# Kernel optimization log

Measured on AMD Instinct MI355X. Metric: run time of the kernel, lower is better.

The kernel has to match this reference:

```python
import jax, jax.numpy as jnp
import numpy as np

B, S, H = 4, 1024, 1024
NH, HD = 16, 64
SCALE = 1.0 / np.sqrt(HD)
VERB_BIAS, ROOT_BIAS, SUFFIX_BIAS = 2.0, 1.5, 1.2
BIG = np.float32(1e9)


def setup_inputs() -> dict:
    key = jax.random.key(0)
    ks = jax.random.split(key, 10)
    inp = {
        "hidden_states": jax.random.normal(ks[0], (B, S, H), dtype=jnp.float32),
        "morpho_types": jax.random.randint(ks[1], (B, S), 0, 5, dtype=jnp.int32),
        # torch Linear: y = x @ W.T + b; store W already transposed as [in, out]
        "Wq": jax.random.normal(ks[2], (H, H), dtype=jnp.float32) * 0.02,
        "bq": jnp.zeros((H,), dtype=jnp.float32),
        "Wk": jax.random.normal(ks[3], (H, H), dtype=jnp.float32) * 0.02,
        "bk": jnp.zeros((H,), dtype=jnp.float32),
        "Wv": jax.random.normal(ks[4], (H, H), dtype=jnp.float32) * 0.02,
        "bv": jnp.zeros((H,), dtype=jnp.float32),
        "Wo": jax.random.normal(ks[5], (H, H), dtype=jnp.float32) * 0.02,
        "bo": jnp.zeros((H,), dtype=jnp.float32),
    }
    return inp


def _morpho_bias(morpho_types):
    """Vectorized equivalent of _create_morpho_bias_mask. Returns [B, S, S]
    (the torch version broadcasts the same bias over all heads)."""
    is_verb = morpho_types == 2                      # [B, S]
    pos = jnp.arange(S)
    dist = jnp.abs(pos[:, None] - pos[None, :])      # [S, S]
    # mask non-verb columns with a huge distance; argmin ties -> smallest j,
    # matching torch's argmin over ascending verb_positions
    dist_m = jnp.where(is_verb[:, None, :], dist[None], BIG)  # [B, S, S]
    nearest = jnp.argmin(dist_m, axis=-1)            # [B, S]
    has_verb = jnp.any(is_verb, axis=-1)             # [B]
    verb_term = VERB_BIAS * jax.nn.one_hot(nearest, S, dtype=jnp.float32)
    verb_term = verb_term * has_verb[:, None, None].astype(jnp.float32)
    col_bias = (ROOT_BIAS * 0.5) * (morpho_types == 0).astype(jnp.float32) \
             + (SUFFIX_BIAS * 0.3) * (morpho_types == 1).astype(jnp.float32)  # [B, S]
    return verb_term + col_bias[:, None, :]          # [B, S, S]


def reference(hidden_states, morpho_types, Wq, bq, Wk, bk, Wv, bv, Wo, bo):
    def proj(W, b):
        y = hidden_states @ W + b                    # [B, S, H]
        return y.reshape(B, S, NH, HD).transpose(0, 2, 1, 3)  # [B, NH, S, HD]

    q = proj(Wq, bq)
    k = proj(Wk, bk)
    v = proj(Wv, bv)

    scores = jnp.einsum('bhqd,bhkd->bhqk', q, k) * SCALE   # [B, NH, S, S]
    scores = scores + _morpho_bias(morpho_types)[:, None]  # broadcast heads

    attn = jax.nn.softmax(scores, axis=-1)
    out = jnp.einsum('bhqk,bhkd->bhqd', attn, v)           # [B, NH, S, HD]
    out = out.transpose(0, 2, 1, 3).reshape(B, S, H)
    return out @ Wo + bo
```

## Files before the change

### kernel.cpp

```cpp
#include <hip/hip_runtime.h>


#define QSCALE 0.18033688011112042f
#define CB0    1.0820212806667225f
#define CB1    0.5193702147200268f
#define VERB2  2.8853900817779268f

typedef float  f32x4   __attribute__((ext_vector_type(4)));
typedef short  s16x8   __attribute__((ext_vector_type(8)));
typedef unsigned short u16x4 __attribute__((ext_vector_type(4)));
typedef unsigned short u16x8 __attribute__((ext_vector_type(8)));

#if __has_builtin(__builtin_amdgcn_exp2f)
#define EXP2F(x) __builtin_amdgcn_exp2f(x)
#else
#define EXP2F(x) exp2f(x)
#endif

__device__ __forceinline__ unsigned short f2bf(float f) {
  union { float f; unsigned u; } a; a.f = f;
  unsigned r = a.u + 0x7fffu + ((a.u >> 16) & 1u);
  return (unsigned short)(r >> 16);
}

__device__ __forceinline__ void async16(const void* g, void* l) {
  __builtin_amdgcn_global_load_lds(
      (const __attribute__((address_space(1))) unsigned int*)g,
      (__attribute__((address_space(3))) unsigned int*)l, 16, 0, 0);
}

__global__ __launch_bounds__(256) void k_prep(
    const float* __restrict__ hs, unsigned short* __restrict__ hsb,
    const float* __restrict__ Wq, const float* __restrict__ Wk,
    const float* __restrict__ Wv, const float* __restrict__ Wo,
    unsigned short* __restrict__ Wt, const int* __restrict__ mt,
    float* __restrict__ colbias, int* __restrict__ nearest) {
  __shared__ float t[64 * 68];
  int bx = blockIdx.x, tid = threadIdx.x;
  if (bx < 2048) {
    int i = (bx * 256 + tid) * 8;
    float4 v0 = *(const float4*)(hs + i);
    float4 v1 = *(const float4*)(hs + i + 4);
    u16x8 o;
    o[0] = f2bf(v0.x); o[1] = f2bf(v0.y); o[2] = f2bf(v0.z); o[3] = f2bf(v0.w);
    o[4] = f2bf(v1.x); o[5] = f2bf(v1.y); o[6] = f2bf(v1.z); o[7] = f2bf(v1.w);
    *(u16x8*)(hsb + i) = o;
  } else if (bx < 3072) {
    int w = (bx - 2048) >> 8, tt = (bx - 2048) & 255;
    const float* W = (w == 0) ? Wq : (w == 1) ? Wk : (w == 2) ? Wv : Wo;
    unsigned short* Wd = Wt + (size_t)w * 1048576;
    int n0 = (tt & 15) * 64, k0 = (tt >> 4) * 64;
    int r = tid >> 2, c0 = (tid & 3) * 16;
    const float* src = &W[(k0 + r) * 1024 + n0 + c0];
    float4 a0 = *(const float4*)(src + 0);
    float4 a1 = *(const float4*)(src + 4);
    float4 a2 = *(const float4*)(src + 8);
    float4 a3 = *(const float4*)(src + 12);
    *(float4*)&t[r * 68 + c0 + 0]  = a0;
    *(float4*)&t[r * 68 + c0 + 4]  = a1;
    *(float4*)&t[r * 68 + c0 + 8]  = a2;
    *(float4*)&t[r * 68 + c0 + 12] = a3;
    __syncthreads();
    u16x8 o0, o1;
#pragma unroll
    for (int j = 0; j < 8; j++) {
      o0[j] = f2bf(t[(c0 + j) * 68 + r]);
      o1[j] = f2bf(t[(c0 + 8 + j) * 68 + r]);
    }
    *(u16x8*)&Wd[(n0 + r) * 1024 + k0 + c0]     = o0;
    *(u16x8*)&Wd[(n0 + r) * 1024 + k0 + c0 + 8] = o1;
  } else {
    int i = bx - 3072;
    int b = i >> 2;
    int* sm = (int*)t;
    for (int j = tid; j < 1024; j += 256) sm[j] = mt[b * 1024 + j];
    __syncthreads();
    int q = (i & 3) * 256 + tid;
    int best = 1 << 30, bj = -1;
    for (int j = 0; j < 1024; ++j) {
      int d = (q > j) ? (q - j) : (j - q);
      int dd = (sm[j] == 2) ? d : (1 << 30);
      if (dd < best) { best = dd; bj = j; }
    }
    nearest[b * 1024 + q] = bj;
    int m = sm[q];
    colbias[b * 1024 + q] = CB0 * (m == 0) + CB1 * (m == 1);
  }
}

template <int MODE>
__global__ __launch_bounds__(256) void k_gemm(
    const unsigned short* __restrict__ A,
    const unsigned short* __restrict__ WtBase,
    const float* __restrict__ bias0, const float* __restrict__ bias1,
    const float* __restrict__ bias2,
    unsigned short* __restrict__ outB, unsigned short* __restrict__ outV,
    float* __restrict__ outF) {
  constexpr int TM = (MODE == 0) ? 128 : 64;
  constexpr int NI = (MODE == 0) ? 4 : 2;
  constexpr int RA = TM / 4;
  __shared__ unsigned short As[TM * 64];
  __shared__ unsigned short Bs[128 * 64];
  int tid = threadIdx.x, wid = tid >> 6, lane = tid & 63;
  int c = lane & 15, quad = lane >> 4;
  int m0, wsel, n0;
  const unsigned short* Bt;
  const float* bias;
  if (MODE == 0) {
    wsel = blockIdx.x >> 3;
    n0 = (blockIdx.x & 7) * 128;
    m0 = blockIdx.y * 128;
    Bt = WtBase + wsel * 1048576;
    bias = (wsel == 0) ? bias0 : ((wsel == 1) ? bias1 : bias2);
  } else {
    wsel = 0;
    n0 = blockIdx.x * 128;
    m0 = blockIdx.y * 64;
    Bt = WtBase; bias = bias0;
  }
  int wm = (wid >> 1) * (16 * NI), wn = (wid & 1) * 64;
  int lr = lane >> 3, lc = lane & 7;
  int gcol = ((lc ^ lr) << 3);
  const unsigned short* ga = A  + (size_t)(m0 + wid * RA + lr) * 1024 + gcol;
  const unsigned short* gb = Bt + (size_t)(n0 + wid * 32 + lr) * 1024 + gcol;
  unsigned short* lA = &As[(wid * RA) * 64];
  unsigned short* lB = &Bs[(wid * 32) * 64];

  f32x4 acc[NI][4];
#pragma unroll
  for (int i = 0; i < NI; i++)
#pragma unroll
    for (int j = 0; j < 4; j++) acc[i][j] = (f32x4){0.f, 0.f, 0.f, 0.f};

  bool sw = (MODE == 1) || (wsel != 2);

  for (int k0 = 0; k0 < 1024; k0 += 64) {
#pragma unroll
    for (int i = 0; i < RA / 8; i++) async16(ga + i * 8 * 1024 + k0, lA + i * 8 * 64);
#pragma unroll
    for (int j = 0; j < 4; j++)      async16(gb + j * 8 * 1024 + k0, lB + j * 8 * 64);
    __syncthreads();
#pragma unroll
    for (int ks = 0; ks < 2; ks++) {
      s16x8 af[NI], bf[4];
#pragma unroll
      for (int i = 0; i < NI; i++)
        af[i] = *(const s16x8*)&As[(wm + i * 16 + c) * 64 + (((ks * 4 + quad) ^ (c & 7)) << 3)];
#pragma unroll
      for (int j = 0; j < 4; j++)
        bf[j] = *(const s16x8*)&Bs[(wn + j * 16 + c) * 64 + (((ks * 4 + quad) ^ (c & 7)) << 3)];
      if (sw) {
#pragma unroll
        for (int i = 0; i < NI; i++)
#pragma unroll
          for (int j = 0; j < 4; j++)
            acc[i][j] = __builtin_amdgcn_mfma_f32_16x16x32_bf16(bf[j], af[i], acc[i][j], 0, 0, 0);
      } else {
#pragma unroll
        for (int i = 0; i < NI; i++)
#pragma unroll
          for (int j = 0; j < 4; j++)
            acc[i][j] = __builtin_amdgcn_mfma_f32_16x16x32_bf16(af[i], bf[j], acc[i][j], 0, 0, 0);
      }
    }
    __syncthreads();
  }

  if (MODE == 1) {
#pragma unroll
    for (int j = 0; j < 4; j++) {
      int colb = n0 + wn + j * 16 + quad * 4;
      f32x4 bvv = *(const f32x4*)&bias[colb];
#pragma unroll
      for (int i = 0; i < NI; i++) {
        int s_tok = m0 + wm + i * 16 + c;
        f32x4 v = acc[i][j] + bvv;
        *(f32x4*)&outF[(size_t)s_tok * 1024 + colb] = v;
      }
    }
  } else if (wsel == 2) {
#pragma unroll
    for (int j = 0; j < 4; j++) {
      int col = n0 + wn + j * 16 + c;
      float bv = bias[col];
      int h = col >> 6, d = col & 63;
#pragma unroll
      for (int i = 0; i < NI; i++) {
        int row = m0 + wm + i * 16 + quad * 4;
        int bb = row >> 10, s = row & 1023;
        u16x4 pk;
#pragma unroll
        for (int r = 0; r < 4; r++) pk[r] = f2bf(acc[i][j][r] + bv);
        *(u16x4*)&outV[(size_t)(((bb * 16 + h) * 64 + d)) * 1024 + s] = pk;
      }
    }
  } else {
    float sc = (wsel == 0) ? QSCALE : 1.0f;
#pragma unroll
    for (int j = 0; j < 4; j++) {
      int colb = n0 + wn + j * 16 + quad * 4;
      f32x4 bvv = *(const f32x4*)&bias[colb];
      int h = colb >> 6, d0 = colb & 63;
#pragma unroll
      for (int i = 0; i < NI; i++) {
        int s_tok = m0 + wm + i * 16 + c;
        int bb = s_tok >> 10, s = s_tok & 1023;
        u16x4 pk;
#pragma unroll
        for (int r = 0; r < 4; r++) pk[r] = f2bf((acc[i][j][r] + bvv[r]) * sc);
        *(u16x4*)&outB[(size_t)wsel * 4194304 + (((bb * 16 + h) * 1024 + s) * 64) + d0] = pk;
      }
    }
  }
}

__global__ __launch_bounds__(256) void k_attn(
    const unsigned short* __restrict__ Q, const unsigned short* __restrict__ K,
    const unsigned short* __restrict__ Vt, const float* __restrict__ colbias,
    const int* __restrict__ nearest, unsigned short* __restrict__ AO) {
  __shared__ unsigned short Ks[64 * 72];
  __shared__ unsigned short Vs[64 * 72];
  __shared__ unsigned short Ps[4][32 * 72];
  __shared__ float Cb[1024];
  int tid = threadIdx.x, wid = tid >> 6, lane = tid & 63;
  int c = lane & 15, quad = lane >> 4;
  int bh = blockIdx.x, qt = blockIdx.y;
  int b = bh >> 4, head = bh & 15;
  int q0 = qt * 128, wq = wid * 32;
  const unsigned short* Qg = Q  + (size_t)(bh * 1024 + q0 + wq) * 64;
  const unsigned short* Kg = K  + (size_t)bh * 1024 * 64;
  const unsigned short* Vg = Vt + (size_t)bh * 64 * 1024;

  *(float4*)&Cb[tid * 4] = *(const float4*)&colbias[b * 1024 + tid * 4];

  s16x8 qf[2][2];
#pragma unroll
  for (int nt = 0; nt < 2; nt++)
#pragma unroll
    for (int ks = 0; ks < 2; ks++)
      qf[nt][ks] = *(const s16x8*)&Qg[(nt * 16 + c) * 64 + ks * 32 + quad * 8];

  int nq[2];
  nq[0] = nearest[b * 1024 + q0 + wq + c];
  nq[1] = nearest[b * 1024 + q0 + wq + 16 + c];

  f32x4 o[2][4];
#pragma unroll
  for (int i = 0; i < 2; i++)
#pragma unroll
    for (int j = 0; j < 4; j++) o[i][j] = (f32x4){0.f, 0.f, 0.f, 0.f};
  float lrun[2] = {0.f, 0.f};

  int srow = tid >> 3, scol8 = (tid & 7) * 8;

  u16x8 kr[2], vr[2];
#pragma unroll
  for (int it = 0; it < 2; ++it) {
    int r2 = it * 32 + srow;
    kr[it] = *(const u16x8*)&Kg[r2 * 64 + scol8];
    vr[it] = *(const u16x8*)&Vg[r2 * 1024 + scol8];
  }
  __syncthreads();

  for (int kc = 0; kc < 16; ++kc) {
#pragma unroll
    for (int it = 0; it < 2; ++it) {
      int r2 = it * 32 + srow;
      *(u16x8*)&Ks[r2 * 72 + scol8] = kr[it];
      *(u16x8*)&Vs[r2 * 72 + scol8] = vr[it];
    }
    __syncthreads();
    if (kc < 15) {
#pragma unroll
      for (int it = 0; it < 2; ++it) {
        int r2 = it * 32 + srow;
        kr[it] = *(const u16x8*)&Kg[((kc + 1) * 64 + r2) * 64 + scol8];
        vr[it] = *(const u16x8*)&Vg[r2 * 1024 + (kc + 1) * 64 + scol8];
      }
    }

    f32x4 st[4][2];
#pragma unroll
    for (int mt = 0; mt < 4; mt++)
#pragma unroll
      for (int nt = 0; nt < 2; nt++) st[mt][nt] = (f32x4){0.f, 0.f, 0.f, 0.f};
#pragma unroll
    for (int mt = 0; mt < 4; mt++)
#pragma unroll
      for (int ks = 0; ks < 2; ks++) {
        s16x8 a = *(const s16x8*)&Ks[(mt * 16 + c) * 72 + ks * 32 + quad * 8];
#pragma unroll
        for (int nt = 0; nt < 2; nt++)
          st[mt][nt] = __builtin_amdgcn_mfma_f32_16x16x32_bf16(a, qf[nt][ks], st[mt][nt], 0, 0, 0);
      }

    bool h0 = (nq[0] >> 6) == kc;
    bool h1 = (nq[1] >> 6) == kc;
    if (__any(h0 || h1)) {
#pragma unroll
      for (int mt = 0; mt < 4; mt++)
#pragma unroll
        for (int nt = 0; nt < 2; nt++)
#pragma unroll
          for (int r = 0; r < 4; r++)
            if (kc * 64 + mt * 16 + quad * 4 + r == nq[nt]) st[mt][nt][r] += VERB2;
    }

#pragma unroll
    for (int mt = 0; mt < 4; mt++) {
      f32x4 cb = *(const f32x4*)&Cb[kc * 64 + mt * 16 + quad * 4];
#pragma unroll
      for (int nt = 0; nt < 2; nt++) {
        float e0 = EXP2F(st[mt][nt][0] + cb[0]);
        float e1 = EXP2F(st[mt][nt][1] + cb[1]);
        float e2 = EXP2F(st[mt][nt][2] + cb[2]);
        float e3 = EXP2F(st[mt][nt][3] + cb[3]);
        unsigned p01 = __builtin_amdgcn_perm(__float_as_uint(e1), __float_as_uint(e0), 0x07060302u);
        unsigned p23 = __builtin_amdgcn_perm(__float_as_uint(e3), __float_as_uint(e2), 0x07060302u);
        lrun[nt] += __uint_as_float(p01 << 16) + __uint_as_float(p01 & 0xffff0000u)
                  + __uint_as_float(p23 << 16) + __uint_as_float(p23 & 0xffff0000u);
        uint2 pk; pk.x = p01; pk.y = p23;
        *(uint2*)&Ps[wid][(nt * 16 + c) * 72 + mt * 16 + quad * 4] = pk;
      }
    }
    __asm__ volatile("s_waitcnt lgkmcnt(0)" ::: "memory");

#pragma unroll
    for (int ks = 0; ks < 2; ks++) {
      s16x8 pa[2];
#pragma unroll
      for (int mtq = 0; mtq < 2; mtq++)
        pa[mtq] = *(const s16x8*)&Ps[wid][(mtq * 16 + c) * 72 + ks * 32 + quad * 8];
#pragma unroll
      for (int ntd = 0; ntd < 4; ntd++) {
        s16x8 vb = *(const s16x8*)&Vs[(ntd * 16 + c) * 72 + ks * 32 + quad * 8];
#pragma unroll
        for (int mtq = 0; mtq < 2; mtq++)
          o[mtq][ntd] = __builtin_amdgcn_mfma_f32_16x16x32_bf16(vb, pa[mtq], o[mtq][ntd], 0, 0, 0);
      }
    }
    __syncthreads();
  }

#pragma unroll
  for (int nt = 0; nt < 2; nt++) {
    lrun[nt] += __shfl_xor(lrun[nt], 16, 64);
    lrun[nt] += __shfl_xor(lrun[nt], 32, 64);
  }
  float linv[2] = {1.0f / lrun[0], 1.0f / lrun[1]};
#pragma unroll
  for (int mtq = 0; mtq < 2; mtq++) {
    size_t row = (size_t)(b * 1024 + q0 + wq + mtq * 16 + c);
#pragma unroll
    for (int ntd = 0; ntd < 4; ntd++) {
      int d0 = ntd * 16 + quad * 4;
      u16x4 pk;
#pragma unroll
      for (int r = 0; r < 4; r++) pk[r] = f2bf(o[mtq][ntd][r] * linv[mtq]);
      *(u16x4*)&AO[row * 1024 + head * 64 + d0] = pk;
    }
  }
}

extern "C" void kernel_launch(void* const* d_in, const int* in_sizes, int n_in,
                              void* d_out, int out_size, void* d_ws, size_t ws_size,
                              hipStream_t stream) {
  const float* hs     = (const float*)d_in[0];
  const int*   morpho = (const int*)d_in[1];
  const float* Wq = (const float*)d_in[2];
  const float* bq = (const float*)d_in[3];
  const float* Wk = (const float*)d_in[4];
  const float* bk = (const float*)d_in[5];
  const float* Wv = (const float*)d_in[6];
  const float* bv = (const float*)d_in[7];
  const float* Wo = (const float*)d_in[8];
  const float* bo = (const float*)d_in[9];
  float* out = (float*)d_out;

  char* ws = (char*)d_ws;
  unsigned short* hsb = (unsigned short*)(ws);
  unsigned short* Wt  = (unsigned short*)(ws + (8u << 20));
  unsigned short* Qb  = (unsigned short*)(ws + (16u << 20));
  unsigned short* Kb  = (unsigned short*)(ws + (24u << 20));
  unsigned short* Vtb = (unsigned short*)(ws + (40u << 20));
  float* colbias      = (float*)(ws + (48u << 20));
  int*   nearestp     = (int*)(ws + (48u << 20) + (16u << 10));
  unsigned short* AO  = hsb;

  k_prep<<<3088, 256, 0, stream>>>(hs, hsb, Wq, Wk, Wv, Wo, Wt, morpho,
                                   colbias, nearestp);
  k_gemm<0><<<dim3(24, 32), 256, 0, stream>>>(hsb, Wt, bq, bk, bv, Qb, Vtb, nullptr);
  k_attn<<<dim3(64, 8), 256, 0, stream>>>(Qb, Kb, Vtb, colbias, nearestp, AO);
  k_gemm<1><<<dim3(8, 64), 256, 0, stream>>>(AO, Wt + 3 * 1048576, bo, nullptr, nullptr,
                                             nullptr, nullptr, out);
  (void)in_sizes; (void)n_in; (void)out_size; (void)ws_size; (void)Kb;
}
```

Baseline: 211.1 us.

## Replace QKV projection GEMM with 256x256-tile 8-wave pipelined kernel

Adds a new QKV projection kernel that uses 256x256 output tiles with 512 threads, double-buffered async global-to-LDS loads with XOR-swizzled layout, and interleaved LDS reads and MFMA quads with barriers and s_setprio. The aim is more data reuse per tile and better overlap of memory traffic with matrix math than the previous 128-wide GEMM. The trade-off is a grid of only 192 blocks, which may underfill the 256 CUs, plus high register pressure from the 8x4 accumulators.

```diff
diff --git a/kernel.cpp b/kernel.cpp
--- a/kernel.cpp
+++ b/kernel.cpp
@@ -214,6 +214,178 @@
   }
 }
 
+#define QKV_QUAD(AFR, MB, NB)                                                 \
+  if (sw) {                                                                   \
+    _Pragma("unroll") for (int ks = 0; ks < 2; ks++)                          \
+    _Pragma("unroll") for (int mf = 0; mf < 4; mf++)                          \
+    _Pragma("unroll") for (int nf = 0; nf < 2; nf++)                          \
+      acc[(MB) + mf][(NB) + nf] = __builtin_amdgcn_mfma_f32_16x16x32_bf16(    \
+          b[(NB) + nf][ks], AFR[mf][ks], acc[(MB) + mf][(NB) + nf], 0, 0, 0); \
+  } else {                                                                    \
+    _Pragma("unroll") for (int ks = 0; ks < 2; ks++)                          \
+    _Pragma("unroll") for (int mf = 0; mf < 4; mf++)                          \
+    _Pragma("unroll") for (int nf = 0; nf < 2; nf++)                          \
+      acc[(MB) + mf][(NB) + nf] = __builtin_amdgcn_mfma_f32_16x16x32_bf16(    \
+          AFR[mf][ks], b[(NB) + nf][ks], acc[(MB) + mf][(NB) + nf], 0, 0, 0); \
+  }
+
+template <bool STAGE, int VMN>
+__device__ __forceinline__ void qkv_ktile(
+    unsigned short* Ac, unsigned short* Bc,
+    const unsigned short* ga, const unsigned short* gb, int k2,
+    int wid, int wm, int wn, int c, int quad, bool sw, f32x4 (&acc)[8][4]) {
+  const int cs = c & 7;
+  s16x8 a0[4][2], a1[4][2], b[4][2];
+#pragma unroll
+  for (int mf = 0; mf < 4; mf++)
+#pragma unroll
+    for (int ks = 0; ks < 2; ks++)
+      a0[mf][ks] = *(const s16x8*)&Ac[(wm * 128 + mf * 16 + c) * 64 + (((ks * 4 + quad) ^ cs) << 3)];
+#pragma unroll
+  for (int nf = 0; nf < 2; nf++)
+#pragma unroll
+    for (int ks = 0; ks < 2; ks++)
+      b[nf][ks] = *(const s16x8*)&Bc[(wn * 64 + nf * 16 + c) * 64 + (((ks * 4 + quad) ^ cs) << 3)];
+  __builtin_amdgcn_s_barrier();
+  __asm__ volatile("s_waitcnt lgkmcnt(0)" ::: "memory");
+  __builtin_amdgcn_s_setprio(1);
+  QKV_QUAD(a0, 0, 0)
+  __builtin_amdgcn_s_setprio(0);
+  __builtin_amdgcn_s_barrier();
+#pragma unroll
+  for (int nf = 2; nf < 4; nf++)
+#pragma unroll
+    for (int ks = 0; ks < 2; ks++)
+      b[nf][ks] = *(const s16x8*)&Bc[(wn * 64 + nf * 16 + c) * 64 + (((ks * 4 + quad) ^ cs) << 3)];
+#pragma unroll
+  for (int mf = 0; mf < 4; mf++)
+#pragma unroll
+    for (int ks = 0; ks < 2; ks++)
+      a1[mf][ks] = *(const s16x8*)&Ac[(wm * 128 + 64 + mf * 16 + c) * 64 + (((ks * 4 + quad) ^ cs) << 3)];
+  __builtin_amdgcn_s_barrier();
+  __asm__ volatile("s_waitcnt lgkmcnt(0)" ::: "memory");
+  __builtin_amdgcn_s_setprio(1);
+  QKV_QUAD(a0, 0, 2)
+  __builtin_amdgcn_s_setprio(0);
+  __builtin_amdgcn_s_barrier();
+  if constexpr (STAGE) {
+#pragma unroll
+    for (int j = 0; j < 2; j++) {
+      async16(ga + j * 8 * 1024 + k2, Ac + (wid * 32 + j * 8) * 64);
+      async16(gb + j * 8 * 1024 + k2, Bc + (wid * 32 + j * 8) * 64);
+    }
+  }
+  __builtin_amdgcn_s_barrier();
+  __builtin_amdgcn_s_setprio(1);
+  QKV_QUAD(a1, 4, 0)
+  __builtin_amdgcn_s_setprio(0);
+  __builtin_amdgcn_s_barrier();
+  if constexpr (STAGE) {
+#pragma unroll
+    for (int j = 2; j < 4; j++) {
+      async16(ga + j * 8 * 1024 + k2, Ac + (wid * 32 + j * 8) * 64);
+      async16(gb + j * 8 * 1024 + k2, Bc + (wid * 32 + j * 8) * 64);
+    }
+  }
+  __builtin_amdgcn_s_barrier();
+  __builtin_amdgcn_s_setprio(1);
+  QKV_QUAD(a1, 4, 2)
+  __builtin_amdgcn_s_setprio(0);
+  if constexpr (VMN == 8)
+    __asm__ volatile("s_waitcnt vmcnt(8)" ::: "memory");
+  else if constexpr (VMN == 0)
+    __asm__ volatile("s_waitcnt vmcnt(0)" ::: "memory");
+  __builtin_amdgcn_s_barrier();
+}
+
+__global__ __launch_bounds__(512, 2) void k_qkv256(
+    const unsigned short* __restrict__ A,
+    const unsigned short* __restrict__ WtBase,
+    const float* __restrict__ bq, const float* __restrict__ bk,
+    const float* __restrict__ bv,
+    unsigned short* __restrict__ outQK, unsigned short* __restrict__ outV) {
+  __shared__ unsigned short As[2][256 * 64];
+  __shared__ unsigned short Bs[2][256 * 64];
+  int tid = threadIdx.x, wid = tid >> 6, lane = tid & 63;
+  int c = lane & 15, quad = lane >> 4;
+  int wm = wid >> 2, wn = wid & 3;
+  int wsel = blockIdx.x >> 2;
+  int n0 = (blockIdx.x & 3) * 256;
+  int m0 = blockIdx.y * 256;
+  const unsigned short* Bt = WtBase + (size_t)wsel * 1048576;
+  const float* bias = (wsel == 0) ? bq : ((wsel == 1) ? bk : bv);
+  bool sw = (wsel != 2);
+
+  int lr = lane >> 3, lc = lane & 7;
+  int gcol = (lc ^ lr) << 3;
+  const unsigned short* ga = A  + (size_t)(m0 + wid * 32 + lr) * 1024 + gcol;
+  const unsigned short* gb = Bt + (size_t)(n0 + wid * 32 + lr) * 1024 + gcol;
+
+  f32x4 acc[8][4];
+#pragma unroll
+  for (int i = 0; i < 8; i++)
+#pragma unroll
+    for (int j = 0; j < 4; j++) acc[i][j] = (f32x4){0.f, 0.f, 0.f, 0.f};
+
+#pragma unroll
+  for (int j = 0; j < 4; j++) {
+    async16(ga + j * 8 * 1024,      &As[0][(wid * 32 + j * 8) * 64]);
+    async16(gb + j * 8 * 1024,      &Bs[0][(wid * 32 + j * 8) * 64]);
+  }
+#pragma unroll
+  for (int j = 0; j < 4; j++) {
+    async16(ga + j * 8 * 1024 + 64, &As[1][(wid * 32 + j * 8) * 64]);
+    async16(gb + j * 8 * 1024 + 64, &Bs[1][(wid * 32 + j * 8) * 64]);
+  }
+  __asm__ volatile("s_waitcnt vmcnt(8)" ::: "memory");
+  __builtin_amdgcn_s_barrier();
+
+  for (int kt = 0; kt < 14; kt += 2) {
+    qkv_ktile<true, 8>(&As[0][0], &Bs[0][0], ga, gb, (kt + 2) * 64,
+                       wid, wm, wn, c, quad, sw, acc);
+    qkv_ktile<true, 8>(&As[1][0], &Bs[1][0], ga, gb, (kt + 3) * 64,
+                       wid, wm, wn, c, quad, sw, acc);
+  }
+  qkv_ktile<false, 0>(&As[0][0], &Bs[0][0], ga, gb, 0, wid, wm, wn, c, quad, sw, acc);
+  qkv_ktile<false, -1>(&As[1][0], &Bs[1][0], ga, gb, 0, wid, wm, wn, c, quad, sw, acc);
+
+  if (!sw) {
+#pragma unroll
+    for (int nf = 0; nf < 4; nf++) {
+      int col = n0 + wn * 64 + nf * 16 + c;
+      float bvv = bias[col];
+      int h = col >> 6, d = col & 63;
+#pragma unroll
+      for (int mf = 0; mf < 8; mf++) {
+        int row = m0 + wm * 128 + mf * 16 + quad * 4;
+        int bb = row >> 10, s = row & 1023;
+        u16x4 pk;
+#pragma unroll
+        for (int r = 0; r < 4; r++) pk[r] = f2bf(acc[mf][nf][r] + bvv);
+        *(u16x4*)&outV[((size_t)(bb * 16 + h) * 64 + d) * 1024 + s] = pk;
+      }
+    }
+  } else {
+    float sc = (wsel == 0) ? QSCALE : 1.0f;
+    unsigned short* outp = outQK + (size_t)wsel * 4194304;
+#pragma unroll
+    for (int nf = 0; nf < 4; nf++) {
+      int colb = n0 + wn * 64 + nf * 16 + quad * 4;
+      f32x4 bvv = *(const f32x4*)&bias[colb];
+      int h = colb >> 6, d0 = colb & 63;
+#pragma unroll
+      for (int mf = 0; mf < 8; mf++) {
+        int tok = m0 + wm * 128 + mf * 16 + c;
+        int bb = tok >> 10, s = tok & 1023;
+        u16x4 pk;
+#pragma unroll
+        for (int r = 0; r < 4; r++) pk[r] = f2bf((acc[mf][nf][r] + bvv[r]) * sc);
+        *(u16x4*)&outp[((size_t)(bb * 16 + h) * 1024 + s) * 64 + d0] = pk;
+      }
+    }
+  }
+}
+
 __global__ __launch_bounds__(256) void k_attn(
     const unsigned short* __restrict__ Q, const unsigned short* __restrict__ K,
     const unsigned short* __restrict__ Vt, const float* __restrict__ colbias,
@@ -389,7 +561,7 @@
 
   k_prep<<<3088, 256, 0, stream>>>(hs, hsb, Wq, Wk, Wv, Wo, Wt, morpho,
                                    colbias, nearestp);
-  k_gemm<0><<<dim3(24, 32), 256, 0, stream>>>(hsb, Wt, bq, bk, bv, Qb, Vtb, nullptr);
+  k_qkv256<<<dim3(12, 16), 512, 0, stream>>>(hsb, Wt, bq, bk, bv, Qb, Vtb);
   k_attn<<<dim3(64, 8), 256, 0, stream>>>(Qb, Kb, Vtb, colbias, nearestp, AO);
   k_gemm<1><<<dim3(8, 64), 256, 0, stream>>>(AO, Wt + 3 * 1048576, bo, nullptr, nullptr,
                                              nullptr, nullptr, out);
```

New measurement: 273.4 us. 29.5% more time.
